# Kernel tuning notes

Measured on AMD Instinct MI355X. Metric: run time of the kernel, lower is better.

The kernel has to match this reference:

```python
import jax, jax.numpy as jnp
import numpy as np

N = 50000          # nodes
E = 800000         # edges (before self loops)
C_IN, HID, C_OUT, L = 128, 64, 64, 3
LSTM_H = (L * HID) // 2   # 96, PyG JK-LSTM hidden size
NEG_SLOPE = 0.2


def gat_conv(x, src, dst, W, a_src, a_dst, b):
    # single-head PyG GATConv
    h = x @ W.T                                  # [N, HID]
    al = h @ a_src                               # [N] src attention logits
    ar = h @ a_dst                               # [N]
    e = jax.nn.leaky_relu(al[src] + ar[dst], NEG_SLOPE)   # [E+N]
    m = jax.ops.segment_max(e, dst, num_segments=N)
    ex = jnp.exp(e - m[dst])
    den = jax.ops.segment_sum(ex, dst, num_segments=N)
    coef = ex / den[dst]                         # segment softmax over dst neighborhoods
    out = jax.ops.segment_sum(coef[:, None] * h[src], dst, num_segments=N)
    return out + b


def lstm_dir(seq, Wih, Whh, bih, bhh, reverse):
    # seq: [L, N, C]; returns hidden states [L, N, H] in original time order
    H = Whh.shape[1]
    h0 = jnp.zeros((seq.shape[1], H), seq.dtype)

    def step(carry, x_t):
        h, c = carry
        g = x_t @ Wih.T + bih + h @ Whh.T + bhh
        i, f, gg, o = jnp.split(g, 4, axis=-1)
        c = jax.nn.sigmoid(f) * c + jax.nn.sigmoid(i) * jnp.tanh(gg)
        h = jax.nn.sigmoid(o) * jnp.tanh(c)
        return (h, c), h

    _, hs = jax.lax.scan(step, (h0, h0), seq, reverse=reverse)
    return hs


def setup_inputs() -> dict:
    key = jax.random.key(0)
    ks = jax.random.split(key, 32)
    s = 0.1
    inp = {
        'x': jax.random.normal(ks[0], (N, C_IN), jnp.float32),
        'edge_index': jax.random.randint(ks[1], (2, E), 0, N, jnp.int64
                                         if jax.config.jax_enable_x64 else jnp.int32),
    }
    dims = [C_IN, HID, HID]
    for l in range(L):
        inp[f'conv{l}_W'] = s * jax.random.normal(ks[2 + 4 * l], (HID, dims[l]), jnp.float32)
        inp[f'conv{l}_asrc'] = s * jax.random.normal(ks[3 + 4 * l], (HID,), jnp.float32)
        inp[f'conv{l}_adst'] = s * jax.random.normal(ks[4 + 4 * l], (HID,), jnp.float32)
        inp[f'conv{l}_b'] = jnp.zeros((HID,), jnp.float32)
    for d, off in (('f', 16), ('b', 20)):
        inp[f'lstm_Wih_{d}'] = s * jax.random.normal(ks[off], (4 * LSTM_H, HID), jnp.float32)
        inp[f'lstm_Whh_{d}'] = s * jax.random.normal(ks[off + 1], (4 * LSTM_H, LSTM_H), jnp.float32)
        inp[f'lstm_bih_{d}'] = jnp.zeros((4 * LSTM_H,), jnp.float32)
        inp[f'lstm_bhh_{d}'] = jnp.zeros((4 * LSTM_H,), jnp.float32)
    inp['att_W'] = s * jax.random.normal(ks[24], (1, 2 * LSTM_H), jnp.float32)
    inp['att_b'] = jnp.zeros((1,), jnp.float32)
    inp['out_W'] = s * jax.random.normal(ks[25], (C_OUT, HID), jnp.float32)
    inp['out_b'] = jnp.zeros((C_OUT,), jnp.float32)
    return inp


def reference(x, edge_index,
              conv0_W, conv0_asrc, conv0_adst, conv0_b,
              conv1_W, conv1_asrc, conv1_adst, conv1_b,
              conv2_W, conv2_asrc, conv2_adst, conv2_b,
              lstm_Wih_f, lstm_Whh_f, lstm_bih_f, lstm_bhh_f,
              lstm_Wih_b, lstm_Whh_b, lstm_bih_b, lstm_bhh_b,
              att_W, att_b, out_W, out_b):
    # add self loops (PyG GATConv default)
    loop = jnp.arange(N, dtype=edge_index.dtype)
    src = jnp.concatenate([edge_index[0], loop])
    dst = jnp.concatenate([edge_index[1], loop])

    convs = [(conv0_W, conv0_asrc, conv0_adst, conv0_b),
             (conv1_W, conv1_asrc, conv1_adst, conv1_b),
             (conv2_W, conv2_asrc, conv2_adst, conv2_b)]
    xs = []
    h = x
    for (W, asrc, adst, b) in convs:
        h = jax.nn.relu(gat_conv(h, src, dst, W, asrc, adst, b))
        xs.append(h)

    seq = jnp.stack(xs, axis=0)                       # [L, N, HID]
    hf = lstm_dir(seq, lstm_Wih_f, lstm_Whh_f, lstm_bih_f, lstm_bhh_f, False)
    hb = lstm_dir(seq, lstm_Wih_b, lstm_Whh_b, lstm_bih_b, lstm_bhh_b, True)
    hcat = jnp.concatenate([hf, hb], axis=-1)         # [L, N, 2*LSTM_H]
    logits = (hcat @ att_W.T + att_b)[..., 0]         # [L, N]
    alpha = jax.nn.softmax(logits, axis=0)            # softmax over layers
    agg = jnp.einsum('lnc,ln->nc', seq, alpha)        # [N, HID]
    return agg @ out_W.T + out_b
```

## Files before the change

### kernel.cpp

```cpp
#include <hip/hip_runtime.h>
#include <hip/hip_bf16.h>
#include <math.h>


typedef __attribute__((ext_vector_type(4))) float f32x4;
typedef __attribute__((ext_vector_type(8))) short bf16x8;

__device__ __forceinline__ float rcp_f(float x) {
    return __builtin_amdgcn_rcpf(x);
}
__device__ __forceinline__ float sigmoid_f(float x) {
    return rcp_f(1.0f + __expf(-x));
}
__device__ __forceinline__ float tanh_f(float x) {
    return fmaf(2.0f, rcp_f(1.0f + __expf(-2.0f * x)), -1.0f);
}
__device__ __forceinline__ unsigned short f2bf(float x) {
    union { float f; unsigned int u; } v; v.f = x;
    unsigned int r = (v.u + 0x7FFFu + ((v.u >> 16) & 1u)) >> 16;
    return (unsigned short)r;
}
__device__ __forceinline__ float bf2f(unsigned short u) {
    union { unsigned int i; float f; } v; v.i = ((unsigned int)u) << 16;
    return v.f;
}

template<int K>
__global__ __launch_bounds__(256) void lin_kernel(
    const float* __restrict__ x, const float* __restrict__ W,
    const float* __restrict__ asrc, const float* __restrict__ adst,
    unsigned short* __restrict__ h, float* __restrict__ al,
    float* __restrict__ ar, int N)
{
    __shared__ __align__(16) float Wl[64][K + 4];
    for (int i = threadIdx.x; i < 64 * K; i += 256)
        Wl[i / K][i % K] = W[i];
    __syncthreads();

    int lane = threadIdx.x & 63;
    float as = asrc[lane], ad = adst[lane];
    int wid = (blockIdx.x * 256 + threadIdx.x) >> 6;
    int nw  = (gridDim.x * 256) >> 6;
    int n4max = (N + 3) >> 2;
    for (int n4 = wid; n4 < n4max; n4 += nw) {
        int nb = __builtin_amdgcn_readfirstlane(n4) << 2;
        const float* xr0 = x + (size_t)nb * K;
        const float* xr1 = x + (size_t)min(nb + 1, N - 1) * K;
        const float* xr2 = x + (size_t)min(nb + 2, N - 1) * K;
        const float* xr3 = x + (size_t)min(nb + 3, N - 1) * K;
        float a0 = 0.f, a1 = 0.f, a2 = 0.f, a3 = 0.f;
        #pragma unroll 4
        for (int k = 0; k < K; k += 4) {
            f32x4 wv = *reinterpret_cast<const f32x4*>(&Wl[lane][k]);
            float4 x0 = *reinterpret_cast<const float4*>(xr0 + k);
            float4 x1 = *reinterpret_cast<const float4*>(xr1 + k);
            float4 x2 = *reinterpret_cast<const float4*>(xr2 + k);
            float4 x3 = *reinterpret_cast<const float4*>(xr3 + k);
            a0 += x0.x * wv.x + x0.y * wv.y + x0.z * wv.z + x0.w * wv.w;
            a1 += x1.x * wv.x + x1.y * wv.y + x1.z * wv.z + x1.w * wv.w;
            a2 += x2.x * wv.x + x2.y * wv.y + x2.z * wv.z + x2.w * wv.w;
            a3 += x3.x * wv.x + x3.y * wv.y + x3.z * wv.z + x3.w * wv.w;
        }
        float accs[4] = {a0, a1, a2, a3};
        #pragma unroll
        for (int j = 0; j < 4; ++j) {
            int n = nb + j;
            if (n >= N) break;
            float acc = accs[j];
            h[(size_t)n * 64 + lane] = f2bf(acc);
            float pa = acc * as, pr = acc * ad;
            #pragma unroll
            for (int off = 32; off > 0; off >>= 1) {
                pa += __shfl_down(pa, off);
                pr += __shfl_down(pr, off);
            }
            if (lane == 0) { al[n] = pa; ar[n] = pr; }
        }
    }
}

__global__ void csr_zero(int* __restrict__ deg, int* __restrict__ cursor, int N)
{
    int i = blockIdx.x * blockDim.x + threadIdx.x;
    if (i < N) { deg[i] = 0; cursor[i] = 0; }
}

__global__ void csr_hist(const int* __restrict__ dst, int* __restrict__ deg, int E)
{
    int i = blockIdx.x * blockDim.x + threadIdx.x;
    if (i < E) atomicAdd(&deg[dst[i]], 1);
}

__global__ void csr_scan1(const int* __restrict__ deg, int* __restrict__ incl,
                          int* __restrict__ part, int N)
{
    __shared__ int sb[2][256];
    int tid = threadIdx.x;
    int i = blockIdx.x * 256 + tid;
    int v = (i < N) ? deg[i] + 1 : 0;
    sb[0][tid] = v;
    __syncthreads();
    int cur = 0;
    #pragma unroll
    for (int off = 1; off < 256; off <<= 1) {
        int s = sb[cur][tid];
        if (tid >= off) s += sb[cur][tid - off];
        sb[cur ^ 1][tid] = s;
        cur ^= 1;
        __syncthreads();
    }
    if (i < N) incl[i] = sb[cur][tid];
    if (tid == 255) part[blockIdx.x] = sb[cur][255];
}

__global__ void csr_scan2(int* __restrict__ part, int NB)
{
    __shared__ int sb[2][256];
    int tid = threadIdx.x;
    int v = (tid < NB) ? part[tid] : 0;
    sb[0][tid] = v;
    __syncthreads();
    int cur = 0;
    #pragma unroll
    for (int off = 1; off < 256; off <<= 1) {
        int s = sb[cur][tid];
        if (tid >= off) s += sb[cur][tid - off];
        sb[cur ^ 1][tid] = s;
        cur ^= 1;
        __syncthreads();
    }
    if (tid < NB) part[tid] = sb[cur][tid] - v;
}

__global__ void csr_scan3(const int* __restrict__ deg, const int* __restrict__ incl,
                          const int* __restrict__ part, int* __restrict__ rowptr,
                          int N, int total)
{
    int i = blockIdx.x * blockDim.x + threadIdx.x;
    if (i < N)
        rowptr[i] = part[i >> 8] + incl[i] - (deg[i] + 1);
    if (i == 0) rowptr[N] = total;
}

__global__ void csr_scatter(const int* __restrict__ src, const int* __restrict__ dst,
                            const int* __restrict__ rowptr, int* __restrict__ cursor,
                            int* __restrict__ csr_src, int E, int N)
{
    int i = blockIdx.x * blockDim.x + threadIdx.x;
    if (i >= E + N) return;
    int s = (i < E) ? src[i] : (i - E);
    int d = (i < E) ? dst[i] : (i - E);
    int pos = atomicAdd(&cursor[d], 1);
    csr_src[rowptr[d] + pos] = s;
}

__global__ __launch_bounds__(256) void agg_kernel(
    const int* __restrict__ rowptr, const int* __restrict__ csr_src,
    const float* __restrict__ al, const float* __restrict__ ar,
    const unsigned short* __restrict__ h, const float* __restrict__ b,
    float* __restrict__ outseq, unsigned short* __restrict__ outseq_bf, int N)
{
    int lane = threadIdx.x & 63;
    int w = threadIdx.x >> 6;
    int d = blockIdx.x * 4 + w;
    if (d >= N) return;
    int li = lane & 15, grp = lane >> 4;

    int rp0 = rowptr[d], rp1 = rowptr[d + 1];
    int degd = rp1 - rp0;
    float ard = ar[d];
    float den = 0.0f;
    float a0 = 0.f, a1 = 0.f, a2 = 0.f, a3 = 0.f;

    for (int c0 = 0; c0 < degd; c0 += 64) {
        int ne = min(64, degd - c0);
        int s_l = 0;
        float ex_l = 0.0f;
        if (lane < ne) {
            s_l = csr_src[rp0 + c0 + lane];
            float e = al[s_l] + ard;
            e = (e >= 0.0f) ? e : 0.2f * e;
            ex_l = __expf(e);
        }
        float dsum = ex_l;
        #pragma unroll
        for (int off = 32; off > 0; off >>= 1) dsum += __shfl_xor(dsum, off);
        den += dsum;
        #pragma unroll 2
        for (int e2 = 0; e2 < ne; e2 += 4) {
            int eA = e2 + grp;
            float exb = __shfl(ex_l, eA);
            int sb = __shfl(s_l, eA);
            uint2 hv = *reinterpret_cast<const uint2*>(
                &h[(size_t)sb * 64 + li * 4]);
            a0 += exb * bf2f((unsigned short)(hv.x & 0xFFFFu));
            a1 += exb * bf2f((unsigned short)(hv.x >> 16));
            a2 += exb * bf2f((unsigned short)(hv.y & 0xFFFFu));
            a3 += exb * bf2f((unsigned short)(hv.y >> 16));
        }
    }
    #pragma unroll
    for (int off = 16; off < 64; off <<= 1) {
        a0 += __shfl_xor(a0, off);
        a1 += __shfl_xor(a1, off);
        a2 += __shfl_xor(a2, off);
        a3 += __shfl_xor(a3, off);
    }
    if (grp == 0) {
        float inv = rcp_f(den);
        int ch = li * 4;
        float4 v;
        v.x = fmaxf(fmaf(a0, inv, b[ch]),     0.0f);
        v.y = fmaxf(fmaf(a1, inv, b[ch + 1]), 0.0f);
        v.z = fmaxf(fmaf(a2, inv, b[ch + 2]), 0.0f);
        v.w = fmaxf(fmaf(a3, inv, b[ch + 3]), 0.0f);
        *reinterpret_cast<float4*>(&outseq[(size_t)d * 64 + ch]) = v;
        uint2 bb;
        bb.x = (unsigned int)f2bf(v.x) | ((unsigned int)f2bf(v.y) << 16);
        bb.y = (unsigned int)f2bf(v.z) | ((unsigned int)f2bf(v.w) << 16);
        *reinterpret_cast<uint2*>(&outseq_bf[(size_t)d * 64 + ch]) = bb;
    }
}

__global__ void prep_lstm(
    const float* __restrict__ WihF, const float* __restrict__ WhhF,
    const float* __restrict__ bihF, const float* __restrict__ bhhF,
    const float* __restrict__ WihB_, const float* __restrict__ WhhB_,
    const float* __restrict__ bihB_, const float* __restrict__ bhhB_,
    unsigned short* __restrict__ WB, float* __restrict__ bsum)
{
    int tid = blockIdx.x * blockDim.x + threadIdx.x;
    if (tid < 2 * 61440) {
        int dir = tid / 61440, rr = tid % 61440;
        const float* Wih = dir ? WihB_ : WihF;
        const float* Whh = dir ? WhhB_ : WhhF;
        float v;
        if (rr < 24576) {
            int f = rr >> 9, l = (rr >> 3) & 63, s = rr & 7;
            int kc = f & 1, qt = f >> 1;
            int q = qt / 6, t6 = qt % 6;
            int j = q * 96 + t6 * 16 + (l & 15);
            int k = kc * 32 + (l >> 4) * 8 + s;
            v = Wih[j * 64 + k];
        } else {
            int rr2 = rr - 24576;
            int f = rr2 >> 9, l = (rr2 >> 3) & 63, s = rr2 & 7;
            int kc = f % 3, qt = f / 3;
            int q = qt / 6, t6 = qt % 6;
            int j = q * 96 + t6 * 16 + (l & 15);
            int k = kc * 32 + (l >> 4) * 8 + s;
            v = Whh[j * 96 + k];
        }
        WB[tid] = f2bf(v);
    } else if (tid < 2 * 61440 + 2 * 384) {
        int q2 = tid - 2 * 61440;
        int dir = q2 / 384, j = q2 % 384;
        bsum[q2] = dir ? (bihB_[j] + bhhB_[j]) : (bihF[j] + bhhF[j]);
    }
}

__global__ __launch_bounds__(768, 3) void lstm_kernel(
    const unsigned short* __restrict__ seq_bf, const float* __restrict__ seq,
    const unsigned short* __restrict__ WB,
    const float* __restrict__ bsum, const float* __restrict__ attW,
    const float* __restrict__ attb, const float* __restrict__ outW,
    const float* __restrict__ outb, float* __restrict__ out, int N)
{
    __shared__ __align__(16) unsigned short smem[81024];
    unsigned short* WL = smem;
    unsigned short* HS = smem + 61440;
    float* LG = reinterpret_cast<float*>(smem + 79872);

    const int tid  = threadIdx.x;
    const int lane = tid & 63;
    const int w    = tid >> 6;
    const int i16  = lane & 15;
    const int g    = lane >> 4;
    const int n0   = blockIdx.x * 192;
    const int nodebase = 16 * w;
    const int myrow = nodebase + g * 4;

    float attb0 = attb[0];
    if (tid < 576) LG[tid] = attb0;

    for (int dir = 0; dir < 2; ++dir) {
        __syncthreads();
        {
            const f32x4* gsrc = reinterpret_cast<const f32x4*>(WB + dir * 61440);
            f32x4* ldst = reinterpret_cast<f32x4*>(WL);
            #pragma unroll
            for (int it = 0; it < 10; ++it)
                ldst[it * 768 + tid] = gsrc[it * 768 + tid];
        }
        {
            unsigned int* hz = reinterpret_cast<unsigned int*>(&HS[nodebase * 96]);
            for (int e2 = lane; e2 < 768; e2 += 64) hz[e2] = 0u;
        }
        const float* bs = bsum + dir * 384;
        const float* aw = attW + dir * 96;
        float bsr[24];
        #pragma unroll
        for (int t6 = 0; t6 < 6; ++t6)
            #pragma unroll
            for (int q = 0; q < 4; ++q)
                bsr[t6 * 4 + q] = bs[q * 96 + t6 * 16 + i16];
        float awr[6];
        #pragma unroll
        for (int t6 = 0; t6 < 6; ++t6) awr[t6] = aw[t6 * 16 + i16];
        float c[24];
        #pragma unroll
        for (int a = 0; a < 24; ++a) c[a] = 0.0f;
        __syncthreads();

        for (int step = 0; step < 3; ++step) {
            int t = dir ? (2 - step) : step;

            int nn = n0 + nodebase + i16;
            nn = (nn < N) ? nn : (N - 1);
            const unsigned short* xr = seq_bf + ((size_t)t * N + nn) * 64 + g * 8;
            bf16x8 ax0 = *reinterpret_cast<const bf16x8*>(xr);
            bf16x8 ax1 = *reinterpret_cast<const bf16x8*>(xr + 32);

            const unsigned short* hrow = &HS[(nodebase + i16) * 96];
            bf16x8 ah0 = *reinterpret_cast<const bf16x8*>(hrow + g * 8);
            bf16x8 ah1 = *reinterpret_cast<const bf16x8*>(hrow + 32 + g * 8);
            bf16x8 ah2 = *reinterpret_cast<const bf16x8*>(hrow + 64 + g * 8);
            const unsigned short* wbase = WL + lane * 8;

            float lp[4] = {0.0f, 0.0f, 0.0f, 0.0f};
            #pragma unroll
            for (int t6 = 0; t6 < 6; ++t6) {
                const int jb = t6 * 16 + i16;
                f32x4 acc4[4];
                #pragma unroll
                for (int q = 0; q < 4; ++q) {
                    float bv = bsr[t6 * 4 + q];
                    acc4[q] = (f32x4){bv, bv, bv, bv};
                }
                #pragma unroll
                for (int q = 0; q < 4; ++q) {
                    const int qt = q * 6 + t6;
                    const unsigned short* wih = wbase + (qt * 2) * 512;
                    const unsigned short* whh = wbase + 24576 + (qt * 3) * 512;
                    acc4[q] = __builtin_amdgcn_mfma_f32_16x16x32_bf16(
                        ax0, *reinterpret_cast<const bf16x8*>(wih), acc4[q], 0, 0, 0);
                    acc4[q] = __builtin_amdgcn_mfma_f32_16x16x32_bf16(
                        ax1, *reinterpret_cast<const bf16x8*>(wih + 512), acc4[q], 0, 0, 0);
                    acc4[q] = __builtin_amdgcn_mfma_f32_16x16x32_bf16(
                        ah0, *reinterpret_cast<const bf16x8*>(whh), acc4[q], 0, 0, 0);
                    acc4[q] = __builtin_amdgcn_mfma_f32_16x16x32_bf16(
                        ah1, *reinterpret_cast<const bf16x8*>(whh + 512), acc4[q], 0, 0, 0);
                    acc4[q] = __builtin_amdgcn_mfma_f32_16x16x32_bf16(
                        ah2, *reinterpret_cast<const bf16x8*>(whh + 1024), acc4[q], 0, 0, 0);
                }
                #pragma unroll
                for (int reg = 0; reg < 4; ++reg) {
                    float ii = acc4[0][reg];
                    float ff = acc4[1][reg];
                    float gg = acc4[2][reg];
                    float oo = acc4[3][reg];
                    float cn = sigmoid_f(ff) * c[t6 * 4 + reg]
                             + sigmoid_f(ii) * tanh_f(gg);
                    c[t6 * 4 + reg] = cn;
                    float hn = sigmoid_f(oo) * tanh_f(cn);
                    HS[(myrow + reg) * 96 + jb] = f2bf(hn);
                    lp[reg] += hn * awr[t6];
                }
            }
            #pragma unroll
            for (int reg = 0; reg < 4; ++reg) {
                float v = lp[reg];
                v += __shfl_xor(v, 1);
                v += __shfl_xor(v, 2);
                v += __shfl_xor(v, 4);
                v += __shfl_xor(v, 8);
                if (i16 == 0) LG[t * 192 + myrow + reg] += v;
            }
        }
    }
    __syncthreads();

    float* alphaF = reinterpret_cast<float*>(HS);
    if (tid < 192) {
        float l0 = LG[tid], l1 = LG[192 + tid], l2 = LG[384 + tid];
        float mx = fmaxf(fmaxf(l0, l1), l2);
        float e0 = __expf(l0 - mx), e1 = __expf(l1 - mx), e2 = __expf(l2 - mx);
        float inv = rcp_f(e0 + e1 + e2);
        alphaF[tid] = e0 * inv; alphaF[192 + tid] = e1 * inv;
        alphaF[384 + tid] = e2 * inv;
    }
    __syncthreads();

    float* aggF = reinterpret_cast<float*>(WL);
    for (int idx = tid; idx < 192 * 64; idx += 768) {
        int r = idx >> 6, k = idx & 63;
        int n = n0 + r;
        float v = 0.0f;
        if (n < N) {
            float a0 = alphaF[r], a1 = alphaF[192 + r], a2 = alphaF[384 + r];
            v = a0 * bf2f(seq_bf[((size_t)n) * 64 + k])
              + a1 * bf2f(seq_bf[((size_t)N + n) * 64 + k])
              + a2 * bf2f(seq_bf[((size_t)2 * N + n) * 64 + k]);
        }
        aggF[r * 68 + k] = v;
    }
    __syncthreads();

    f32x4 ow[16];
    #pragma unroll
    for (int kk = 0; kk < 16; ++kk)
        ow[kk] = *reinterpret_cast<const f32x4*>(&outW[(size_t)lane * 64 + kk * 4]);
    float ob = outb[lane];
    for (int r = w; r < 192; r += 12) {
        int n = n0 + r;
        if (n >= N) break;
        float a = ob;
        #pragma unroll
        for (int kk = 0; kk < 16; ++kk) {
            f32x4 av = *reinterpret_cast<const f32x4*>(&aggF[r * 68 + kk * 4]);
            a += ow[kk].x * av.x + ow[kk].y * av.y
               + ow[kk].z * av.z + ow[kk].w * av.w;
        }
        out[(size_t)n * 64 + lane] = a;
    }
}

extern "C" void kernel_launch(void* const* d_in, const int* in_sizes, int n_in,
                              void* d_out, int out_size, void* d_ws, size_t ws_size,
                              hipStream_t stream)
{
    const float* x    = (const float*)d_in[0];
    const int*   ei   = (const int*)d_in[1];
    const float* convW[3]  = {(const float*)d_in[2], (const float*)d_in[6],  (const float*)d_in[10]};
    const float* convAs[3] = {(const float*)d_in[3], (const float*)d_in[7],  (const float*)d_in[11]};
    const float* convAd[3] = {(const float*)d_in[4], (const float*)d_in[8],  (const float*)d_in[12]};
    const float* convB[3]  = {(const float*)d_in[5], (const float*)d_in[9],  (const float*)d_in[13]};
    const float* WihF = (const float*)d_in[14];
    const float* WhhF = (const float*)d_in[15];
    const float* bihF = (const float*)d_in[16];
    const float* bhhF = (const float*)d_in[17];
    const float* WihB = (const float*)d_in[18];
    const float* WhhB = (const float*)d_in[19];
    const float* bihB = (const float*)d_in[20];
    const float* bhhB = (const float*)d_in[21];
    const float* attW = (const float*)d_in[22];
    const float* attb = (const float*)d_in[23];
    const float* outW = (const float*)d_in[24];
    const float* outb = (const float*)d_in[25];

    int N = in_sizes[0] / 128;
    int E = in_sizes[1] / 2;
    const int* src = ei;
    const int* dst = ei + E;
    int total = E + N;

    float* w = (float*)d_ws;
    float* seq  = w;  w += (size_t)3 * N * 64;
    unsigned short* h_bf = (unsigned short*)w;  w += (size_t)N * 32;
    float* al   = w;  w += N;
    float* ar   = w;  w += N;
    float* bsum = w;  w += 768;
    unsigned short* WB = (unsigned short*)w;  w += 61440;
    unsigned short* seq_bf = (unsigned short*)w;  w += (size_t)3 * N * 32;
    int* deg     = (int*)w;        w += N;
    int* cursor  = (int*)w;        w += N;
    int* rowptr  = (int*)w;        w += (N + 1);
    int* incl    = (int*)w;        w += N;
    int* part    = (int*)w;        w += 256;
    int* csr_src = (int*)w;        w += total;

    int NB = (N + 255) / 256;

    csr_zero<<<NB, 256, 0, stream>>>(deg, cursor, N);
    csr_hist<<<(E + 255) / 256, 256, 0, stream>>>(dst, deg, E);
    csr_scan1<<<NB, 256, 0, stream>>>(deg, incl, part, N);
    csr_scan2<<<1, 256, 0, stream>>>(part, NB);
    csr_scan3<<<NB, 256, 0, stream>>>(deg, incl, part, rowptr, N, total);
    csr_scatter<<<(total + 255) / 256, 256, 0, stream>>>(src, dst, rowptr, cursor,
                                                         csr_src, E, N);

    prep_lstm<<<(2 * 61440 + 768 + 255) / 256, 256, 0, stream>>>(
        WihF, WhhF, bihF, bhhF, WihB, WhhB, bihB, bhhB, WB, bsum);

    for (int l = 0; l < 3; ++l) {
        const float* in = (l == 0) ? x : seq + (size_t)(l - 1) * N * 64;
        if (l == 0)
            lin_kernel<128><<<2048, 256, 0, stream>>>(in, convW[l], convAs[l], convAd[l],
                                                      h_bf, al, ar, N);
        else
            lin_kernel<64><<<2048, 256, 0, stream>>>(in, convW[l], convAs[l], convAd[l],
                                                     h_bf, al, ar, N);
        agg_kernel<<<(N + 3) / 4, 256, 0, stream>>>(rowptr, csr_src, al, ar, h_bf,
                                                    convB[l], seq + (size_t)l * N * 64,
                                                    seq_bf + (size_t)l * N * 64, N);
    }

    lstm_kernel<<<(N + 191) / 192, 768, 0, stream>>>(seq_bf, seq, WB, bsum, attW, attb,
                                                     outW, outb, (float*)d_out, N);
}
```

Baseline: 440.4 us.

## Make LSTM kernel persistent with per-wave tiles and split JK epilogue into separate kernel

The LSTM kernel becomes a persistent grid of 256 blocks. Each wave processes up to two 16-node tiles and keeps logits in registers, so the weights are staged into LDS once per block instead of once per 192 nodes. Each wave gets its own padded hidden-state buffer (row stride 104) to reduce LDS bank conflicts. The softmax-over-layers, aggregation and output projection move to a new jk_kernel that uses wave shuffles, at the cost of an extra launch and a global round-trip for the logits.

```diff
diff --git a/kernel.cpp b/kernel.cpp
--- a/kernel.cpp
+++ b/kernel.cpp
@@ -259,29 +259,29 @@
     }
 }
 
-__global__ __launch_bounds__(768, 3) void lstm_kernel(
-    const unsigned short* __restrict__ seq_bf, const float* __restrict__ seq,
+__global__ __launch_bounds__(768) __attribute__((amdgpu_waves_per_eu(3)))
+void lstm_kernel(
+    const unsigned short* __restrict__ seq_bf,
     const unsigned short* __restrict__ WB,
     const float* __restrict__ bsum, const float* __restrict__ attW,
-    const float* __restrict__ attb, const float* __restrict__ outW,
-    const float* __restrict__ outb, float* __restrict__ out, int N)
-{
-    __shared__ __align__(16) unsigned short smem[81024];
+    const float* __restrict__ attb, float* __restrict__ logitG, int N)
+{
+    __shared__ __align__(16) unsigned short smem[81408];
     unsigned short* WL = smem;
-    unsigned short* HS = smem + 61440;
-    float* LG = reinterpret_cast<float*>(smem + 79872);
 
     const int tid  = threadIdx.x;
     const int lane = tid & 63;
     const int w    = tid >> 6;
     const int i16  = lane & 15;
     const int g    = lane >> 4;
-    const int n0   = blockIdx.x * 192;
-    const int nodebase = 16 * w;
-    const int myrow = nodebase + g * 4;
-
-    float attb0 = attb[0];
-    if (tid < 576) LG[tid] = attb0;
+    unsigned short* HSw = smem + 61440 + w * (16 * 104);
+    const int wglob = w * 256 + blockIdx.x;
+    const int tiles_total = (N + 15) >> 4;
+    const float attb0 = attb[0];
+
+    float la[24];
+    #pragma unroll
+    for (int a = 0; a < 24; ++a) la[a] = 0.0f;
 
     for (int dir = 0; dir < 2; ++dir) {
         __syncthreads();
@@ -292,10 +292,6 @@
             for (int it = 0; it < 10; ++it)
                 ldst[it * 768 + tid] = gsrc[it * 768 + tid];
         }
-        {
-            unsigned int* hz = reinterpret_cast<unsigned int*>(&HS[nodebase * 96]);
-            for (int e2 = lane; e2 < 768; e2 += 64) hz[e2] = 0u;
-        }
         const float* bs = bsum + dir * 384;
         const float* aw = attW + dir * 96;
         float bsr[24];
@@ -307,121 +303,136 @@
         float awr[6];
         #pragma unroll
         for (int t6 = 0; t6 < 6; ++t6) awr[t6] = aw[t6 * 16 + i16];
-        float c[24];
-        #pragma unroll
-        for (int a = 0; a < 24; ++a) c[a] = 0.0f;
         __syncthreads();
 
-        for (int step = 0; step < 3; ++step) {
-            int t = dir ? (2 - step) : step;
-
-            int nn = n0 + nodebase + i16;
-            nn = (nn < N) ? nn : (N - 1);
-            const unsigned short* xr = seq_bf + ((size_t)t * N + nn) * 64 + g * 8;
-            bf16x8 ax0 = *reinterpret_cast<const bf16x8*>(xr);
-            bf16x8 ax1 = *reinterpret_cast<const bf16x8*>(xr + 32);
-
-            const unsigned short* hrow = &HS[(nodebase + i16) * 96];
-            bf16x8 ah0 = *reinterpret_cast<const bf16x8*>(hrow + g * 8);
-            bf16x8 ah1 = *reinterpret_cast<const bf16x8*>(hrow + 32 + g * 8);
-            bf16x8 ah2 = *reinterpret_cast<const bf16x8*>(hrow + 64 + g * 8);
-            const unsigned short* wbase = WL + lane * 8;
-
-            float lp[4] = {0.0f, 0.0f, 0.0f, 0.0f};
+        #pragma unroll
+        for (int pass = 0; pass < 2; ++pass) {
+            int tile = pass * 3072 + wglob;
+            if (tile >= tiles_total) continue;
+
+            for (int e2 = lane; e2 < 768; e2 += 64) {
+                int r = e2 / 48, cdw = e2 % 48;
+                *reinterpret_cast<unsigned int*>(&HSw[r * 104 + cdw * 2]) = 0u;
+            }
+            float c[24];
             #pragma unroll
-            for (int t6 = 0; t6 < 6; ++t6) {
-                const int jb = t6 * 16 + i16;
-                f32x4 acc4[4];
+            for (int a = 0; a < 24; ++a) c[a] = 0.0f;
+
+            #pragma unroll
+            for (int step = 0; step < 3; ++step) {
+                int t = dir ? (2 - step) : step;
+                int nn = tile * 16 + i16;
+                nn = (nn < N) ? nn : (N - 1);
+                const unsigned short* xr = seq_bf + ((size_t)t * N + nn) * 64 + g * 8;
+                bf16x8 ax0 = *reinterpret_cast<const bf16x8*>(xr);
+                bf16x8 ax1 = *reinterpret_cast<const bf16x8*>(xr + 32);
+                const unsigned short* hrow = &HSw[i16 * 104];
+                bf16x8 ah0 = *reinterpret_cast<const bf16x8*>(hrow + g * 8);
+                bf16x8 ah1 = *reinterpret_cast<const bf16x8*>(hrow + 32 + g * 8);
+                bf16x8 ah2 = *reinterpret_cast<const bf16x8*>(hrow + 64 + g * 8);
+                const unsigned short* wbase = WL + lane * 8;
+
+                float lp[4] = {0.0f, 0.0f, 0.0f, 0.0f};
                 #pragma unroll
-                for (int q = 0; q < 4; ++q) {
-                    float bv = bsr[t6 * 4 + q];
-                    acc4[q] = (f32x4){bv, bv, bv, bv};
+                for (int t6 = 0; t6 < 6; ++t6) {
+                    const int jb = t6 * 16 + i16;
+                    f32x4 acc4[4];
+                    #pragma unroll
+                    for (int q = 0; q < 4; ++q) {
+                        float bv = bsr[t6 * 4 + q];
+                        acc4[q] = (f32x4){bv, bv, bv, bv};
+                    }
+                    #pragma unroll
+                    for (int q = 0; q < 4; ++q) {
+                        const int qt = q * 6 + t6;
+                        const unsigned short* wih = wbase + (qt * 2) * 512;
+                        const unsigned short* whh = wbase + 24576 + (qt * 3) * 512;
+                        acc4[q] = __builtin_amdgcn_mfma_f32_16x16x32_bf16(
+                            ax0, *reinterpret_cast<const bf16x8*>(wih), acc4[q], 0, 0, 0);
+                        acc4[q] = __builtin_amdgcn_mfma_f32_16x16x32_bf16(
+                            ax1, *reinterpret_cast<const bf16x8*>(wih + 512), acc4[q], 0, 0, 0);
+                        acc4[q] = __builtin_amdgcn_mfma_f32_16x16x32_bf16(
+                            ah0, *reinterpret_cast<const bf16x8*>(whh), acc4[q], 0, 0, 0);
+                        acc4[q] = __builtin_amdgcn_mfma_f32_16x16x32_bf16(
+                            ah1, *reinterpret_cast<const bf16x8*>(whh + 512), acc4[q], 0, 0, 0);
+                        acc4[q] = __builtin_amdgcn_mfma_f32_16x16x32_bf16(
+                            ah2, *reinterpret_cast<const bf16x8*>(whh + 1024), acc4[q], 0, 0, 0);
+                    }
+                    #pragma unroll
+                    for (int reg = 0; reg < 4; ++reg) {
+                        float ii = acc4[0][reg];
+                        float ff = acc4[1][reg];
+                        float gg = acc4[2][reg];
+                        float oo = acc4[3][reg];
+                        float cn = sigmoid_f(ff) * c[t6 * 4 + reg]
+                                 + sigmoid_f(ii) * tanh_f(gg);
+                        c[t6 * 4 + reg] = cn;
+                        float hn = sigmoid_f(oo) * tanh_f(cn);
+                        HSw[(g * 4 + reg) * 104 + jb] = f2bf(hn);
+                        lp[reg] += hn * awr[t6];
+                    }
                 }
                 #pragma unroll
-                for (int q = 0; q < 4; ++q) {
-                    const int qt = q * 6 + t6;
-                    const unsigned short* wih = wbase + (qt * 2) * 512;
-                    const unsigned short* whh = wbase + 24576 + (qt * 3) * 512;
-                    acc4[q] = __builtin_amdgcn_mfma_f32_16x16x32_bf16(
-                        ax0, *reinterpret_cast<const bf16x8*>(wih), acc4[q], 0, 0, 0);
-                    acc4[q] = __builtin_amdgcn_mfma_f32_16x16x32_bf16(
-                        ax1, *reinterpret_cast<const bf16x8*>(wih + 512), acc4[q], 0, 0, 0);
-                    acc4[q] = __builtin_amdgcn_mfma_f32_16x16x32_bf16(
-                        ah0, *reinterpret_cast<const bf16x8*>(whh), acc4[q], 0, 0, 0);
-                    acc4[q] = __builtin_amdgcn_mfma_f32_16x16x32_bf16(
-                        ah1, *reinterpret_cast<const bf16x8*>(whh + 512), acc4[q], 0, 0, 0);
-                    acc4[q] = __builtin_amdgcn_mfma_f32_16x16x32_bf16(
-                        ah2, *reinterpret_cast<const bf16x8*>(whh + 1024), acc4[q], 0, 0, 0);
-                }
-                #pragma unroll
-                for (int reg = 0; reg < 4; ++reg) {
-                    float ii = acc4[0][reg];
-                    float ff = acc4[1][reg];
-                    float gg = acc4[2][reg];
-                    float oo = acc4[3][reg];
-                    float cn = sigmoid_f(ff) * c[t6 * 4 + reg]
-                             + sigmoid_f(ii) * tanh_f(gg);
-                    c[t6 * 4 + reg] = cn;
-                    float hn = sigmoid_f(oo) * tanh_f(cn);
-                    HS[(myrow + reg) * 96 + jb] = f2bf(hn);
-                    lp[reg] += hn * awr[t6];
-                }
+                for (int reg = 0; reg < 4; ++reg)
+                    la[pass * 12 + t * 4 + reg] += lp[reg];
             }
+        }
+    }
+
+    #pragma unroll
+    for (int pass = 0; pass < 2; ++pass) {
+        int tile = pass * 3072 + wglob;
+        if (tile >= tiles_total) continue;
+        #pragma unroll
+        for (int t = 0; t < 3; ++t)
             #pragma unroll
             for (int reg = 0; reg < 4; ++reg) {
-                float v = lp[reg];
+                float v = la[pass * 12 + t * 4 + reg];
                 v += __shfl_xor(v, 1);
                 v += __shfl_xor(v, 2);
                 v += __shfl_xor(v, 4);
                 v += __shfl_xor(v, 8);
-                if (i16 == 0) LG[t * 192 + myrow + reg] += v;
+                int n = tile * 16 + g * 4 + reg;
+                if (i16 == 0 && n < N)
+                    logitG[(size_t)t * N + n] = v + attb0;
             }
-        }
-    }
-    __syncthreads();
-
-    float* alphaF = reinterpret_cast<float*>(HS);
-    if (tid < 192) {
-        float l0 = LG[tid], l1 = LG[192 + tid], l2 = LG[384 + tid];
-        float mx = fmaxf(fmaxf(l0, l1), l2);
-        float e0 = __expf(l0 - mx), e1 = __expf(l1 - mx), e2 = __expf(l2 - mx);
-        float inv = rcp_f(e0 + e1 + e2);
-        alphaF[tid] = e0 * inv; alphaF[192 + tid] = e1 * inv;
-        alphaF[384 + tid] = e2 * inv;
-    }
-    __syncthreads();
-
-    float* aggF = reinterpret_cast<float*>(WL);
-    for (int idx = tid; idx < 192 * 64; idx += 768) {
-        int r = idx >> 6, k = idx & 63;
-        int n = n0 + r;
-        float v = 0.0f;
-        if (n < N) {
-            float a0 = alphaF[r], a1 = alphaF[192 + r], a2 = alphaF[384 + r];
-            v = a0 * bf2f(seq_bf[((size_t)n) * 64 + k])
-              + a1 * bf2f(seq_bf[((size_t)N + n) * 64 + k])
-              + a2 * bf2f(seq_bf[((size_t)2 * N + n) * 64 + k]);
-        }
-        aggF[r * 68 + k] = v;
-    }
-    __syncthreads();
+    }
+}
+
+__global__ __launch_bounds__(256) void jk_kernel(
+    const float* __restrict__ logitG, const unsigned short* __restrict__ seq_bf,
+    const float* __restrict__ outW, const float* __restrict__ outb,
+    float* __restrict__ out, int N)
+{
+    int lane = threadIdx.x & 63;
+    int w = threadIdx.x >> 6;
 
     f32x4 ow[16];
     #pragma unroll
     for (int kk = 0; kk < 16; ++kk)
         ow[kk] = *reinterpret_cast<const f32x4*>(&outW[(size_t)lane * 64 + kk * 4]);
     float ob = outb[lane];
-    for (int r = w; r < 192; r += 12) {
-        int n = n0 + r;
-        if (n >= N) break;
-        float a = ob;
-        #pragma unroll
-        for (int kk = 0; kk < 16; ++kk) {
-            f32x4 av = *reinterpret_cast<const f32x4*>(&aggF[r * 68 + kk * 4]);
-            a += ow[kk].x * av.x + ow[kk].y * av.y
-               + ow[kk].z * av.z + ow[kk].w * av.w;
-        }
-        out[(size_t)n * 64 + lane] = a;
+
+    for (int n = blockIdx.x * 4 + w; n < N; n += gridDim.x * 4) {
+        int nu = __builtin_amdgcn_readfirstlane(n);
+        float l0 = logitG[nu], l1 = logitG[N + nu], l2 = logitG[2 * (size_t)N + nu];
+        float mx = fmaxf(fmaxf(l0, l1), l2);
+        float e0 = __expf(l0 - mx), e1 = __expf(l1 - mx), e2 = __expf(l2 - mx);
+        float inv = rcp_f(e0 + e1 + e2);
+        float a0 = e0 * inv, a1 = e1 * inv, a2 = e2 * inv;
+        float aggk = a0 * bf2f(seq_bf[(size_t)nu * 64 + lane])
+                   + a1 * bf2f(seq_bf[((size_t)N + nu) * 64 + lane])
+                   + a2 * bf2f(seq_bf[((size_t)2 * N + nu) * 64 + lane]);
+        float acc = ob;
+        #pragma unroll
+        for (int k = 0; k < 64; ++k) {
+            float av = __shfl(aggk, k);
+            float wv = (k & 3) == 0 ? ow[k >> 2].x :
+                       (k & 3) == 1 ? ow[k >> 2].y :
+                       (k & 3) == 2 ? ow[k >> 2].z : ow[k >> 2].w;
+            acc = fmaf(av, wv, acc);
+        }
+        out[(size_t)nu * 64 + lane] = acc;
     }
 }
 
@@ -462,6 +473,7 @@
     float* bsum = w;  w += 768;
     unsigned short* WB = (unsigned short*)w;  w += 61440;
     unsigned short* seq_bf = (unsigned short*)w;  w += (size_t)3 * N * 32;
+    float* logitG = w;  w += (size_t)3 * N;
     int* deg     = (int*)w;        w += N;
     int* cursor  = (int*)w;        w += N;
     int* rowptr  = (int*)w;        w += (N + 1);
@@ -495,6 +507,6 @@
                                                     seq_bf + (size_t)l * N * 64, N);
     }
 
-    lstm_kernel<<<(N + 191) / 192, 768, 0, stream>>>(seq_bf, seq, WB, bsum, attW, attb,
-                                                     outW, outb, (float*)d_out, N);
-}
+    lstm_kernel<<<256, 768, 0, stream>>>(seq_bf, WB, bsum, attW, attb, logitG, N);
+    jk_kernel<<<2048, 256, 0, stream>>>(logitG, seq_bf, outW, outb, (float*)d_out, N);
+}
```

After: 563.4 us. 27.9% more time.
